# Kernel tuning notes

Hardware: AMD Instinct MI355X
Metric: run time of the kernel (lower is better)

Reference implementation:

```python
import jax, jax.numpy as jnp
import numpy as np

D_MODEL = 512
NUM_HEADS = 8
D_QKV = D_MODEL // NUM_HEADS  # 64
CAPACITY = 2  # EUNN tunable-style rotation layers per step
B = 2
L = 256


def setup_inputs() -> dict:
    key = jax.random.key(0)
    ks = jax.random.split(key, 16)
    f = jnp.float32
    x_q = jax.random.normal(ks[0], (B, L, D_MODEL), f)
    x_k = jax.random.normal(ks[1], (B, L, D_MODEL), f)
    x_v = jax.random.normal(ks[2], (B, L, D_MODEL), f)
    mask = jnp.zeros((B, 1, L, L), f)
    s = 1.0 / np.sqrt(D_MODEL).astype(np.float32)
    Wq = jax.random.normal(ks[3], (D_MODEL, D_MODEL), f) * s
    Wk = jax.random.normal(ks[4], (D_MODEL, D_MODEL), f) * s
    Wv = jax.random.normal(ks[5], (D_MODEL, D_MODEL), f) * s
    Wo = jax.random.normal(ks[6], (D_MODEL, D_MODEL), f) * s
    bq = jnp.zeros((D_MODEL,), f); bk = jnp.zeros((D_MODEL,), f)
    bv = jnp.zeros((D_MODEL,), f); bo = jnp.zeros((D_MODEL,), f)
    pi = np.float32(np.pi)
    theta = jax.random.uniform(ks[7], (NUM_HEADS, CAPACITY, D_QKV // 2), f, -pi, pi)
    phi = jax.random.uniform(ks[8], (NUM_HEADS, CAPACITY, D_QKV // 2), f, -pi, pi)
    sw = 1.0 / np.sqrt(D_QKV).astype(np.float32)
    Win_re = jax.random.normal(ks[9], (NUM_HEADS, D_QKV, D_QKV), f) * sw
    Win_im = jax.random.normal(ks[10], (NUM_HEADS, D_QKV, D_QKV), f) * sw
    rnn_bias = jax.random.normal(ks[11], (NUM_HEADS, D_QKV), f) * 0.01
    return dict(x_q=x_q, x_k=x_k, x_v=x_v, mask=mask, Wq=Wq, bq=bq, Wk=Wk, bk=bk,
                Wv=Wv, bv=bv, Wo=Wo, bo=bo, theta=theta, phi=phi,
                Win_re=Win_re, Win_im=Win_im, rnn_bias=rnn_bias)


def _apply_unitary(h, theta, phi):
    # h: [B,H,Q,d] complex64. EUNN unitary = product of Givens-rotation layers,
    # alternating even pairings (0,1),(2,3),.. and odd pairings via roll.
    for c in range(theta.shape[1]):
        if c % 2 == 1:
            h = jnp.roll(h, -1, axis=-1)
        sh = h.shape
        hp = h.reshape(sh[:-1] + (sh[-1] // 2, 2))
        a, b = hp[..., 0], hp[..., 1]
        cs = jnp.cos(theta[:, c, :])[None, :, None, :]
        sn = jnpp_sin = jnp.sin(theta[:, c, :])[None, :, None, :]
        ph = jnp.exp(1j * phi[:, c, :].astype(jnp.complex64))[None, :, None, :]
        na = cs * a - (sn * ph) * b
        nb = (sn * jnp.conj(ph)) * a + cs * b
        h = jnp.stack([na, nb], axis=-1).reshape(sh)
        if c % 2 == 1:
            h = jnp.roll(h, 1, axis=-1)
    return h


def _modrelu(z, b):
    m = jnp.abs(z)
    scale = jax.nn.relu(m + b) / (m + 1e-5)
    return z * scale.astype(z.dtype)


def _forward(x_q, x_k, x_v, mask, Wq, bq, Wk, bk, Wv, bv, Wo, bo,
             theta, phi, Win_re, Win_im, rnn_bias):
    Bm, Lq, _ = x_q.shape
    def heads(x):
        return x.reshape(Bm, -1, NUM_HEADS, D_QKV).transpose(0, 2, 1, 3)
    q = heads(x_q @ Wq + bq)   # [B,H,Lq,d]
    k = heads(x_k @ Wk + bk)   # [B,H,Lk,d]
    v = heads(x_v @ Wv + bv)   # [B,H,Lk,d]
    logits = jnp.einsum('bhqd,bhkd->bhqk', q, k) / jnp.sqrt(jnp.float32(D_QKV))
    logits = logits - jnp.where(mask == 1.0, jnp.inf, mask)
    attn = jax.nn.softmax(logits, axis=-1)  # [B,H,Lq,Lk]
    Win = (Win_re + 1j * Win_im).astype(jnp.complex64)  # [H,d,d]
    bb = rnn_bias[None, :, None, :]
    def step(h, xs):
        a_t, v_t = xs                              # [B,H,Q], [B,H,d]
        x_t = a_t[..., None] * v_t[:, :, None, :]  # [B,H,Q,d] streamed weighted value
        wx = jnp.einsum('bhqd,hde->bhqe', x_t.astype(jnp.complex64), Win)
        return _modrelu(_apply_unitary(h, theta, phi) + wx, bb), None
    h0 = jnp.zeros((Bm, NUM_HEADS, Lq, D_QKV), jnp.complex64)
    xs = (attn.transpose(3, 0, 1, 2), v.transpose(2, 0, 1, 3))
    hT, _ = jax.lax.scan(step, h0, xs)
    rnn_out = jnp.real(hT)  # [B,H,Lq,d] -- TF takes final RNN state, real part
    out = rnn_out.transpose(0, 2, 1, 3).reshape(Bm, Lq, D_MODEL) @ Wo + bo
    return out, attn


def reference(x_q, x_k, x_v, mask, Wq, bq, Wk, bk, Wv, bv, Wo, bo,
              theta, phi, Win_re, Win_im, rnn_bias):
    return _forward(x_q, x_k, x_v, mask, Wq, bq, Wk, bk, Wv, bv, Wo, bo,
                    theta, phi, Win_re, Win_im, rnn_bias)
```

## Files before the change

### kernel.cpp

```cpp
#include <hip/hip_runtime.h>
#include <math.h>

#define NB 2
#define NL 256
#define DM 512
#define NH 8
#define DQ 64

typedef float v2f __attribute__((ext_vector_type(2)));

#if __has_builtin(__builtin_elementwise_fma)
__device__ __forceinline__ v2f fmav(v2f a, v2f b, v2f c) {
    return __builtin_elementwise_fma(a, b, c);
}
#else
__device__ __forceinline__ v2f fmav(v2f a, v2f b, v2f c) {
    v2f r; r.x = fmaf(a.x, b.x, c.x); r.y = fmaf(a.y, b.y, c.y); return r;
}
#endif
__device__ __forceinline__ v2f swapv(v2f a) {
    return __builtin_shufflevector(a, a, 1, 0);
}

__global__ __launch_bounds__(256) void qkv_gemm(
    const float* __restrict__ xq, const float* __restrict__ xk,
    const float* __restrict__ xv,
    const float* __restrict__ Wq, const float* __restrict__ Wk,
    const float* __restrict__ Wv,
    const float* __restrict__ bq, const float* __restrict__ bk,
    const float* __restrict__ bv,
    const float* __restrict__ Wre, const float* __restrict__ Wim,
    float* __restrict__ q, float* __restrict__ kT, float2* __restrict__ u)
{
    int z = blockIdx.z;
    const float* X = (z == 0) ? xq : (z == 1) ? xk : xv;
    const float* W = (z == 0) ? Wq : (z == 1) ? Wk : Wv;
    const float* bias = (z == 0) ? bq : (z == 1) ? bk : bv;

    __shared__ float As[32][33];
    __shared__ float Bs[32][68];

    int tid = threadIdx.x;
    int tx = tid & 15, ty = tid >> 4;
    int m0 = blockIdx.y * 32, n0 = blockIdx.x * 64;

    int ar = tid >> 3, ac4 = (tid & 7) * 4;
    int br = tid >> 4, bc4 = (tid & 15) * 4;
    const float* Aptr = X + (m0 + ar) * 512 + ac4;
    const float* Bptr0 = W + br * 512 + n0 + bc4;
    const float* Bptr1 = W + (br + 16) * 512 + n0 + bc4;

    float acc[2][4] = {};

    float4 aR = *(const float4*)(Aptr);
    float4 bR0 = *(const float4*)(Bptr0);
    float4 bR1 = *(const float4*)(Bptr1);

    for (int k0 = 0; k0 < 512; k0 += 32) {
        As[ac4 + 0][ar] = aR.x; As[ac4 + 1][ar] = aR.y;
        As[ac4 + 2][ar] = aR.z; As[ac4 + 3][ar] = aR.w;
        *(float4*)&Bs[br][bc4] = bR0;
        *(float4*)&Bs[br + 16][bc4] = bR1;
        __syncthreads();

        if (k0 + 32 < 512) {
            aR  = *(const float4*)(Aptr + k0 + 32);
            bR0 = *(const float4*)(Bptr0 + (k0 + 32) * 512);
            bR1 = *(const float4*)(Bptr1 + (k0 + 32) * 512);
        }

        #pragma unroll
        for (int kk = 0; kk < 32; kk++) {
            float a0 = As[kk][ty * 2 + 0];
            float a1 = As[kk][ty * 2 + 1];
            float4 bb = *(const float4*)&Bs[kk][tx * 4];
            acc[0][0] += a0 * bb.x; acc[0][1] += a0 * bb.y;
            acc[0][2] += a0 * bb.z; acc[0][3] += a0 * bb.w;
            acc[1][0] += a1 * bb.x; acc[1][1] += a1 * bb.y;
            acc[1][2] += a1 * bb.z; acc[1][3] += a1 * bb.w;
        }
        __syncthreads();
    }

    if (z < 2) {
        float* O = (z == 0) ? q : kT;
        #pragma unroll
        for (int i = 0; i < 2; i++) {
            int m = m0 + ty * 2 + i;
            int b = m >> 8, l = m & 255;
            #pragma unroll
            for (int j = 0; j < 4; j++) {
                int n = n0 + tx * 4 + j;
                int h = n >> 6, d = n & 63;
                float val = acc[i][j] + bias[n];
                if (z == 1)
                    O[((b * NH + h) * DQ + d) * NL + l] = val;
                else
                    O[((b * NH + h) * NL + l) * DQ + d] = val;
            }
        }
    } else {
        int h = blockIdx.x;
        int b = m0 >> 8;
        #pragma unroll
        for (int i = 0; i < 2; i++)
            #pragma unroll
            for (int j = 0; j < 4; j++)
                Bs[ty * 2 + i][tx * 4 + j] = acc[i][j] + bias[n0 + tx * 4 + j];
        __syncthreads();

        int r0 = ty * 2, c4 = tx * 4;
        float ur[2][4] = {}, ui[2][4] = {};
        const float* wr = Wre + h * 4096 + c4;
        const float* wi = Wim + h * 4096 + c4;
        #pragma unroll 4
        for (int d = 0; d < 64; d++) {
            float v0 = Bs[r0][d];
            float v1 = Bs[r0 + 1][d];
            float4 wre = *(const float4*)(wr + d * 64);
            float4 wim = *(const float4*)(wi + d * 64);
            ur[0][0] += v0 * wre.x; ur[0][1] += v0 * wre.y;
            ur[0][2] += v0 * wre.z; ur[0][3] += v0 * wre.w;
            ui[0][0] += v0 * wim.x; ui[0][1] += v0 * wim.y;
            ui[0][2] += v0 * wim.z; ui[0][3] += v0 * wim.w;
            ur[1][0] += v1 * wre.x; ur[1][1] += v1 * wre.y;
            ur[1][2] += v1 * wre.z; ur[1][3] += v1 * wre.w;
            ui[1][0] += v1 * wim.x; ui[1][1] += v1 * wim.y;
            ui[1][2] += v1 * wim.z; ui[1][3] += v1 * wim.w;
        }
        #pragma unroll
        for (int i = 0; i < 2; i++) {
            int l = (m0 & 255) + r0 + i;
            float2* up = u + ((size_t)(b * NH + h) * NL + l) * DQ + c4;
            #pragma unroll
            for (int j = 0; j < 4; j++)
                up[j] = make_float2(ur[i][j], ui[i][j]);
        }
    }
}

__device__ __forceinline__ float dpp_swap1(float x) {
    return __int_as_float(__builtin_amdgcn_mov_dpp(__float_as_int(x), 0xB1, 0xF, 0xF, true));
}
__device__ __forceinline__ float dpp_rol1(float x) {
    return __int_as_float(__builtin_amdgcn_mov_dpp(__float_as_int(x), 0x134, 0xF, 0xF, true));
}
__device__ __forceinline__ float dpp_ror1(float x) {
    return __int_as_float(__builtin_amdgcn_mov_dpp(__float_as_int(x), 0x13C, 0xF, 0xF, true));
}

__global__ __launch_bounds__(256) void rnn_kernel(
    const float* __restrict__ q, const float* __restrict__ kT,
    const float* __restrict__ mask, float* __restrict__ attn_o,
    const float2* __restrict__ u,
    const float* __restrict__ theta, const float* __restrict__ phi,
    const float* __restrict__ rnn_bias, float* __restrict__ rnn_out)
{
    int tid  = threadIdx.x;
    int wv   = tid >> 6;
    int lane = tid & 63;

    int blk = blockIdx.x;
    int qg  = blk & 63;
    int h   = (blk >> 6) & 7;
    int b   = blk >> 9;

    __shared__ float qs[256];
    __shared__ float lg[4 * 260];
    __shared__ float redm[4], reds[4];
    __shared__ float arow[4 * 256];

    {
        qs[tid] = q[((size_t)(b * NH + h) * NL + qg * 4) * DQ + tid];
        __syncthreads();

        const float* kp = kT + (size_t)((b * NH + h) * DQ) * NL + tid;
        float acc[4] = {};
        #pragma unroll
        for (int d4 = 0; d4 < 16; d4++) {
            float kv0 = kp[(d4 * 4 + 0) * NL];
            float kv1 = kp[(d4 * 4 + 1) * NL];
            float kv2 = kp[(d4 * 4 + 2) * NL];
            float kv3 = kp[(d4 * 4 + 3) * NL];
            #pragma unroll
            for (int j = 0; j < 4; j++) {
                const float4 qv = *(const float4*)&qs[j * 64 + d4 * 4];
                acc[j] += qv.x * kv0 + qv.y * kv1 + qv.z * kv2 + qv.w * kv3;
            }
        }
        #pragma unroll
        for (int j = 0; j < 4; j++) {
            float mv = mask[(size_t)(b * NL + qg * 4 + j) * NL + tid];
            acc[j] = acc[j] * 0.125f - ((mv == 1.0f) ? INFINITY : mv);
            lg[j * 260 + tid] = acc[j];
        }
        __syncthreads();
        {
            int j = wv;
            float v0 = lg[j * 260 + lane],       v1 = lg[j * 260 + 64 + lane];
            float v2 = lg[j * 260 + 128 + lane], v3 = lg[j * 260 + 192 + lane];
            float mx = fmaxf(fmaxf(v0, v1), fmaxf(v2, v3));
            #pragma unroll
            for (int o = 32; o; o >>= 1) mx = fmaxf(mx, __shfl_xor(mx, o, 64));
            float s = __expf(v0 - mx) + __expf(v1 - mx) +
                      __expf(v2 - mx) + __expf(v3 - mx);
            #pragma unroll
            for (int o = 32; o; o >>= 1) s += __shfl_xor(s, o, 64);
            if (lane == 0) { redm[j] = mx; reds[j] = s; }
        }
        __syncthreads();
        #pragma unroll
        for (int j = 0; j < 4; j++) {
            float p = __expf(acc[j] - redm[j]) * __builtin_amdgcn_rcpf(reds[j]);
            attn_o[((size_t)(b * NH + h) * NL + qg * 4 + j) * NL + tid] = p;
            arow[j * 256 + tid] = p;
        }
        __syncthreads();
    }

    int d = lane;
    bool odd = d & 1;

    const float* tb = theta + h * 64;
    const float* pb = phi + h * 64;

    int i0 = d >> 1;
    float th0 = tb[i0], ph0 = pb[i0];
    float c0 = cosf(th0), s0 = sinf(th0);
    float W0r = (odd ? s0 : -s0) * cosf(ph0);
    float W0i = -s0 * sinf(ph0);

    int i1 = odd ? (d >> 1) : (((d + 62) & 63) >> 1);
    float th1 = tb[32 + i1], ph1 = pb[32 + i1];
    float c1 = cosf(th1), s1 = sinf(th1);
    float W1r = (odd ? -s1 : s1) * cosf(ph1);
    float W1i = -s1 * sinf(ph1);

    float biasv = rnn_bias[h * 64 + d];

    v2f c0v = {c0, c0}, c1v = {c1, c1};
    v2f W0rV = {W0r, W0r}, W0iN = {-W0i, W0i};
    v2f W1rV = {W1r, W1r}, W1iN = {-W1i, W1i};

    const float* arc = arow + wv * 256;
    const float2* up = u + (size_t)((b * NH + h) * NL) * DQ + d;

    v2f e = {0.f, 0.f};
    #pragma unroll 8
    for (int t = 0; t < 256; t++) {
        float2 uu = up[t * 64];
        float a_t = arc[t];
        v2f atv = {a_t, a_t};
        v2f uv = {uu.x, uu.y};

        v2f p0;
        p0.x = dpp_swap1(e.x); p0.y = dpp_swap1(e.y);
        v2f g = fmav(c0v, e, fmav(W0rV, p0, W0iN * swapv(p0)));

        v2f rl, rr;
        rl.x = dpp_rol1(g.x); rl.y = dpp_rol1(g.y);
        rr.x = dpp_ror1(g.x); rr.y = dpp_ror1(g.y);
        v2f p1;
        p1.x = odd ? rl.x : rr.x;
        p1.y = odd ? rl.y : rr.y;

        v2f z = fmav(c1v, g, fmav(W1rV, p1, fmav(W1iN, swapv(p1), atv * uv)));

        float mm = z.x * z.x + z.y * z.y;
        float m = __builtin_amdgcn_sqrtf(mm);
        float sc = fmaxf(m + biasv, 0.f) * __builtin_amdgcn_rcpf(m + 1e-5f);
        v2f scv = {sc, sc};
        e = z * scv;
    }

    int qi = qg * 4 + wv;
    rnn_out[(size_t)(b * NL + qi) * DM + h * DQ + d] = e.x;
}

__global__ __launch_bounds__(256) void out_gemm(
    const float* __restrict__ A, const float* __restrict__ W,
    const float* __restrict__ bias, float* __restrict__ C)
{
    __shared__ float As[32][17];
    __shared__ float Bs[32][68];

    int tid = threadIdx.x;
    int tx = tid & 15, ty = tid >> 4;
    int m0 = blockIdx.y * 16, n0 = blockIdx.x * 64;

    int ar = tid >> 4, ac2 = (tid & 15) * 2;
    int br = tid >> 4, bc4 = (tid & 15) * 4;
    const float* Aptr = A + (m0 + ar) * 512 + ac2;
    const float* Bptr0 = W + br * 512 + n0 + bc4;
    const float* Bptr1 = W + (br + 16) * 512 + n0 + bc4;

    float acc[4] = {};

    float2 aR = *(const float2*)(Aptr);
    float4 bR0 = *(const float4*)(Bptr0);
    float4 bR1 = *(const float4*)(Bptr1);

    for (int k0 = 0; k0 < 512; k0 += 32) {
        As[ac2 + 0][ar] = aR.x; As[ac2 + 1][ar] = aR.y;
        *(float4*)&Bs[br][bc4] = bR0;
        *(float4*)&Bs[br + 16][bc4] = bR1;
        __syncthreads();

        if (k0 + 32 < 512) {
            aR  = *(const float2*)(Aptr + k0 + 32);
            bR0 = *(const float4*)(Bptr0 + (k0 + 32) * 512);
            bR1 = *(const float4*)(Bptr1 + (k0 + 32) * 512);
        }

        #pragma unroll
        for (int kk = 0; kk < 32; kk++) {
            float a = As[kk][ty];
            float4 bb = *(const float4*)&Bs[kk][tx * 4];
            acc[0] += a * bb.x; acc[1] += a * bb.y;
            acc[2] += a * bb.z; acc[3] += a * bb.w;
        }
        __syncthreads();
    }

    int m = m0 + ty;
    #pragma unroll
    for (int j = 0; j < 4; j++) {
        int n = n0 + tx * 4 + j;
        C[m * 512 + n] = acc[j] + bias[n];
    }
}

extern "C" void kernel_launch(void* const* d_in, const int* in_sizes, int n_in,
                              void* d_out, int out_size, void* d_ws, size_t ws_size,
                              hipStream_t stream)
{
    const float* x_q  = (const float*)d_in[0];
    const float* x_k  = (const float*)d_in[1];
    const float* x_v  = (const float*)d_in[2];
    const float* mask = (const float*)d_in[3];
    const float* Wq   = (const float*)d_in[4];
    const float* bq   = (const float*)d_in[5];
    const float* Wk   = (const float*)d_in[6];
    const float* bk   = (const float*)d_in[7];
    const float* Wv   = (const float*)d_in[8];
    const float* bv   = (const float*)d_in[9];
    const float* Wo   = (const float*)d_in[10];
    const float* bo   = (const float*)d_in[11];
    const float* theta= (const float*)d_in[12];
    const float* phi  = (const float*)d_in[13];
    const float* Wre  = (const float*)d_in[14];
    const float* Wim  = (const float*)d_in[15];
    const float* rb   = (const float*)d_in[16];

    float* ws = (float*)d_ws;
    float*  q_ws    = ws;
    float*  kT_ws   = ws + 262144;
    float2* u_ws    = (float2*)(ws + 524288);
    float*  rnn_o   = ws + 1048576;

    float* out_o  = (float*)d_out;
    float* attn_o = out_o + NB * NL * DM;

    qkv_gemm<<<dim3(8, 16, 3), 256, 0, stream>>>(
        x_q, x_k, x_v, Wq, Wk, Wv, bq, bk, bv, Wre, Wim,
        q_ws, kT_ws, u_ws);

    rnn_kernel<<<dim3(1024), 256, 0, stream>>>(
        q_ws, kT_ws, mask, attn_o, u_ws, theta, phi, rb, rnn_o);

    out_gemm<<<dim3(8, 32), 256, 0, stream>>>(rnn_o, Wo, bo, out_o);
}
```

Measured before the change: 188.5 us.

## Pack four hidden dims per lane in RNN scan with 64-thread blocks

The RNN kernel now uses one 64-lane wavefront per block, and each lane holds four consecutive hidden dimensions of one query row (16 lanes per row, 4 rows per wave). The first Givens layer becomes purely in-register, so only one row-rotate DPP per boundary is needed instead of the previous swap plus two rotates. The attention softmax is computed by the single wave with no cross-wave reductions. Per-step u values and attention weights are double-buffered as float4 register loads to hide latency. The cost is fewer threads per CU (256 threads become 64 per block) and more registers per lane, so occupancy and latency hiding depend on how many blocks fit.

```diff
diff --git a/kernel.cpp b/kernel.cpp
--- a/kernel.cpp
+++ b/kernel.cpp
@@ -139,142 +139,183 @@
     }
 }
 
-__device__ __forceinline__ float dpp_swap1(float x) {
-    return __int_as_float(__builtin_amdgcn_mov_dpp(__float_as_int(x), 0xB1, 0xF, 0xF, true));
-}
-__device__ __forceinline__ float dpp_rol1(float x) {
-    return __int_as_float(__builtin_amdgcn_mov_dpp(__float_as_int(x), 0x134, 0xF, 0xF, true));
-}
-__device__ __forceinline__ float dpp_ror1(float x) {
-    return __int_as_float(__builtin_amdgcn_mov_dpp(__float_as_int(x), 0x13C, 0xF, 0xF, true));
-}
-
-__global__ __launch_bounds__(256) void rnn_kernel(
+__device__ __forceinline__ float dpp_row_ror1(float x) {
+    return __int_as_float(__builtin_amdgcn_mov_dpp(__float_as_int(x), 0x121, 0xF, 0xF, true));
+}
+__device__ __forceinline__ float dpp_row_rol1(float x) {
+    return __int_as_float(__builtin_amdgcn_mov_dpp(__float_as_int(x), 0x12F, 0xF, 0xF, true));
+}
+
+__device__ __forceinline__ v2f mdr(v2f z, float bv) {
+    float mm = z.x * z.x + z.y * z.y;
+    float m = __builtin_amdgcn_sqrtf(mm);
+    float sc = fmaxf(m + bv, 0.f) * __builtin_amdgcn_rcpf(m + 1e-5f);
+    v2f s = {sc, sc};
+    return z * s;
+}
+
+__global__ __launch_bounds__(64) void rnn_kernel(
     const float* __restrict__ q, const float* __restrict__ kT,
     const float* __restrict__ mask, float* __restrict__ attn_o,
     const float2* __restrict__ u,
     const float* __restrict__ theta, const float* __restrict__ phi,
     const float* __restrict__ rnn_bias, float* __restrict__ rnn_out)
 {
-    int tid  = threadIdx.x;
-    int wv   = tid >> 6;
-    int lane = tid & 63;
-
+    int lane = threadIdx.x;
     int blk = blockIdx.x;
-    int qg  = blk & 63;
-    int h   = (blk >> 6) & 7;
-    int b   = blk >> 9;
-
-    __shared__ float qs[256];
-    __shared__ float lg[4 * 260];
-    __shared__ float redm[4], reds[4];
-    __shared__ float arow[4 * 256];
+    int qg = blk & 63;
+    int h  = (blk >> 6) & 7;
+    int b  = blk >> 9;
+
+    int row = lane >> 4;
+    int p   = lane & 15;
+
+    __shared__ float qs[4][68];
+    __shared__ float arow[4][260];
 
     {
-        qs[tid] = q[((size_t)(b * NH + h) * NL + qg * 4) * DQ + tid];
-        __syncthreads();
-
-        const float* kp = kT + (size_t)((b * NH + h) * DQ) * NL + tid;
-        float acc[4] = {};
+        const float4* qsrc = (const float4*)(q + ((size_t)(b * NH + h) * NL + qg * 4) * DQ);
+        float4 f4 = qsrc[lane];
+        *(float4*)&qs[lane >> 4][(lane & 15) * 4] = f4;
+    }
+    __syncthreads();
+
+    float l[4][4];
+    {
+        const float* kp = kT + (size_t)((b * NH + h) * DQ) * NL + lane;
+        float acc[4][4] = {};
         #pragma unroll
         for (int d4 = 0; d4 < 16; d4++) {
-            float kv0 = kp[(d4 * 4 + 0) * NL];
-            float kv1 = kp[(d4 * 4 + 1) * NL];
-            float kv2 = kp[(d4 * 4 + 2) * NL];
-            float kv3 = kp[(d4 * 4 + 3) * NL];
-            #pragma unroll
-            for (int j = 0; j < 4; j++) {
-                const float4 qv = *(const float4*)&qs[j * 64 + d4 * 4];
-                acc[j] += qv.x * kv0 + qv.y * kv1 + qv.z * kv2 + qv.w * kv3;
+            float kv[4][4];
+            #pragma unroll
+            for (int kk = 0; kk < 4; kk++)
+                #pragma unroll
+                for (int i = 0; i < 4; i++)
+                    kv[kk][i] = kp[(size_t)(d4 * 4 + i) * NL + kk * 64];
+            #pragma unroll
+            for (int r = 0; r < 4; r++) {
+                float4 qv = *(const float4*)&qs[r][d4 * 4];
+                #pragma unroll
+                for (int kk = 0; kk < 4; kk++)
+                    acc[r][kk] += qv.x * kv[kk][0] + qv.y * kv[kk][1]
+                                + qv.z * kv[kk][2] + qv.w * kv[kk][3];
             }
         }
         #pragma unroll
-        for (int j = 0; j < 4; j++) {
-            float mv = mask[(size_t)(b * NL + qg * 4 + j) * NL + tid];
-            acc[j] = acc[j] * 0.125f - ((mv == 1.0f) ? INFINITY : mv);
-            lg[j * 260 + tid] = acc[j];
-        }
-        __syncthreads();
-        {
-            int j = wv;
-            float v0 = lg[j * 260 + lane],       v1 = lg[j * 260 + 64 + lane];
-            float v2 = lg[j * 260 + 128 + lane], v3 = lg[j * 260 + 192 + lane];
-            float mx = fmaxf(fmaxf(v0, v1), fmaxf(v2, v3));
+        for (int r = 0; r < 4; r++)
+            #pragma unroll
+            for (int kk = 0; kk < 4; kk++) {
+                float mv = mask[(size_t)(b * NL + qg * 4 + r) * NL + lane + kk * 64];
+                l[r][kk] = acc[r][kk] * 0.125f - ((mv == 1.0f) ? INFINITY : mv);
+            }
+        #pragma unroll
+        for (int r = 0; r < 4; r++) {
+            float mx = fmaxf(fmaxf(l[r][0], l[r][1]), fmaxf(l[r][2], l[r][3]));
             #pragma unroll
             for (int o = 32; o; o >>= 1) mx = fmaxf(mx, __shfl_xor(mx, o, 64));
-            float s = __expf(v0 - mx) + __expf(v1 - mx) +
-                      __expf(v2 - mx) + __expf(v3 - mx);
+            float s = __expf(l[r][0] - mx) + __expf(l[r][1] - mx)
+                    + __expf(l[r][2] - mx) + __expf(l[r][3] - mx);
             #pragma unroll
             for (int o = 32; o; o >>= 1) s += __shfl_xor(s, o, 64);
-            if (lane == 0) { redm[j] = mx; reds[j] = s; }
-        }
-        __syncthreads();
-        #pragma unroll
-        for (int j = 0; j < 4; j++) {
-            float p = __expf(acc[j] - redm[j]) * __builtin_amdgcn_rcpf(reds[j]);
-            attn_o[((size_t)(b * NH + h) * NL + qg * 4 + j) * NL + tid] = p;
-            arow[j * 256 + tid] = p;
-        }
-        __syncthreads();
-    }
-
-    int d = lane;
-    bool odd = d & 1;
+            float rs = __builtin_amdgcn_rcpf(s);
+            #pragma unroll
+            for (int kk = 0; kk < 4; kk++) {
+                float pv = __expf(l[r][kk] - mx) * rs;
+                attn_o[((size_t)(b * NH + h) * NL + qg * 4 + r) * NL + lane + kk * 64] = pv;
+                arow[r][lane + kk * 64] = pv;
+            }
+        }
+    }
+    __syncthreads();
 
     const float* tb = theta + h * 64;
     const float* pb = phi + h * 64;
 
-    int i0 = d >> 1;
-    float th0 = tb[i0], ph0 = pb[i0];
-    float c0 = cosf(th0), s0 = sinf(th0);
-    float W0r = (odd ? s0 : -s0) * cosf(ph0);
-    float W0i = -s0 * sinf(ph0);
-
-    int i1 = odd ? (d >> 1) : (((d + 62) & 63) >> 1);
-    float th1 = tb[32 + i1], ph1 = pb[32 + i1];
-    float c1 = cosf(th1), s1 = sinf(th1);
-    float W1r = (odd ? -s1 : s1) * cosf(ph1);
-    float W1i = -s1 * sinf(ph1);
-
-    float biasv = rnn_bias[h * 64 + d];
-
-    v2f c0v = {c0, c0}, c1v = {c1, c1};
-    v2f W0rV = {W0r, W0r}, W0iN = {-W0i, W0i};
-    v2f W1rV = {W1r, W1r}, W1iN = {-W1i, W1i};
-
-    const float* arc = arow + wv * 256;
-    const float2* up = u + (size_t)((b * NH + h) * NL) * DQ + d;
-
-    v2f e = {0.f, 0.f};
-    #pragma unroll 8
-    for (int t = 0; t < 256; t++) {
-        float2 uu = up[t * 64];
-        float a_t = arc[t];
-        v2f atv = {a_t, a_t};
-        v2f uv = {uu.x, uu.y};
-
-        v2f p0;
-        p0.x = dpp_swap1(e.x); p0.y = dpp_swap1(e.y);
-        v2f g = fmav(c0v, e, fmav(W0rV, p0, W0iN * swapv(p0)));
-
-        v2f rl, rr;
-        rl.x = dpp_rol1(g.x); rl.y = dpp_rol1(g.y);
-        rr.x = dpp_ror1(g.x); rr.y = dpp_ror1(g.y);
-        v2f p1;
-        p1.x = odd ? rl.x : rr.x;
-        p1.y = odd ? rl.y : rr.y;
-
-        v2f z = fmav(c1v, g, fmav(W1rV, p1, fmav(W1iN, swapv(p1), atv * uv)));
-
-        float mm = z.x * z.x + z.y * z.y;
-        float m = __builtin_amdgcn_sqrtf(mm);
-        float sc = fmaxf(m + biasv, 0.f) * __builtin_amdgcn_rcpf(m + 1e-5f);
-        v2f scv = {sc, sc};
-        e = z * scv;
-    }
-
-    int qi = qg * 4 + wv;
-    rnn_out[(size_t)(b * NL + qi) * DM + h * DQ + d] = e.x;
+    float thA = tb[2 * p], phA = pb[2 * p];
+    float cA = cosf(thA), sA = sinf(thA), cpA = cosf(phA), spA = sinf(phA);
+    float thB = tb[2 * p + 1], phB = pb[2 * p + 1];
+    float cB = cosf(thB), sB = sinf(thB), cpB = cosf(phB), spB = sinf(phB);
+
+    #define MKC(nm, Wr, Wi) v2f nm##rV = {(Wr), (Wr)}; v2f nm##iN = {-(Wi), (Wi)}
+    MKC(WAa, -sA * cpA, -sA * spA);
+    MKC(WAb,  sA * cpA, -sA * spA);
+    MKC(WBa, -sB * cpB, -sB * spB);
+    MKC(WBb,  sB * cpB, -sB * spB);
+    v2f cAv = {cA, cA}, cBv = {cB, cB};
+
+    int iL = (2 * p + 31) & 31;
+    float thL = tb[32 + iL], phL = pb[32 + iL];
+    float cL = cosf(thL), sL = sinf(thL);
+    MKC(W1L,  sL * cosf(phL), -sL * sinf(phL));
+    float thM = tb[32 + 2 * p], phM = pb[32 + 2 * p];
+    float cM = cosf(thM), sM = sinf(thM), cpM = cosf(phM), spM = sinf(phM);
+    MKC(W1M, -sM * cpM, -sM * spM);
+    MKC(W2M,  sM * cpM, -sM * spM);
+    float thR = tb[32 + 2 * p + 1], phR = pb[32 + 2 * p + 1];
+    float cR = cosf(thR), sR = sinf(thR);
+    MKC(W1R, -sR * cosf(phR), -sR * sinf(phR));
+    v2f cLv = {cL, cL}, cMv = {cM, cM}, cRv = {cR, cR};
+    #undef MKC
+
+    float4 bias4 = *(const float4*)&rnn_bias[h * 64 + 4 * p];
+
+    v2f e0 = {0.f, 0.f}, e1 = {0.f, 0.f}, e2 = {0.f, 0.f}, e3 = {0.f, 0.f};
+
+    #define STEP(a_t, uA, uB) do {                                           \
+        v2f atv = {(a_t), (a_t)};                                            \
+        v2f u0 = {(uA).x, (uA).y}, u1 = {(uA).z, (uA).w};                    \
+        v2f u2 = {(uB).x, (uB).y}, u3 = {(uB).z, (uB).w};                    \
+        v2f g0 = fmav(cAv, e0, fmav(WAarV, e1, WAaiN * swapv(e1)));          \
+        v2f g1 = fmav(cAv, e1, fmav(WAbrV, e0, WAbiN * swapv(e0)));          \
+        v2f g2 = fmav(cBv, e2, fmav(WBarV, e3, WBaiN * swapv(e3)));          \
+        v2f g3 = fmav(cBv, e3, fmav(WBbrV, e2, WBbiN * swapv(e2)));          \
+        v2f gl, gr;                                                          \
+        gl.x = dpp_row_ror1(g3.x); gl.y = dpp_row_ror1(g3.y);                \
+        gr.x = dpp_row_rol1(g0.x); gr.y = dpp_row_rol1(g0.y);                \
+        v2f z0 = fmav(cLv, g0, fmav(W1LrV, gl, fmav(W1LiN, swapv(gl), atv * u0))); \
+        v2f z1 = fmav(cMv, g1, fmav(W1MrV, g2, fmav(W1MiN, swapv(g2), atv * u1))); \
+        v2f z2 = fmav(cMv, g2, fmav(W2MrV, g1, fmav(W2MiN, swapv(g1), atv * u2))); \
+        v2f z3 = fmav(cRv, g3, fmav(W1RrV, gr, fmav(W1RiN, swapv(gr), atv * u3))); \
+        e0 = mdr(z0, bias4.x); e1 = mdr(z1, bias4.y);                        \
+        e2 = mdr(z2, bias4.z); e3 = mdr(z3, bias4.w);                        \
+    } while (0)
+
+    const float4* up4 = (const float4*)(u + (size_t)((b * NH + h) * NL) * DQ) + 2 * p;
+
+    float4 Ua[8], Ub[8];
+    float4 aa, ab;
+    #pragma unroll
+    for (int i = 0; i < 8; i++) Ua[i] = up4[(i >> 1) * 32 + (i & 1)];
+    aa = *(const float4*)&arow[row][0];
+
+    for (int c = 0; c < 64; c += 2) {
+        const float4* upn = up4 + (c + 1) * 128;
+        #pragma unroll
+        for (int i = 0; i < 8; i++) Ub[i] = upn[(i >> 1) * 32 + (i & 1)];
+        ab = *(const float4*)&arow[row][(c + 1) * 4];
+
+        STEP(aa.x, Ua[0], Ua[1]);
+        STEP(aa.y, Ua[2], Ua[3]);
+        STEP(aa.z, Ua[4], Ua[5]);
+        STEP(aa.w, Ua[6], Ua[7]);
+
+        if (c + 2 < 64) {
+            const float4* upn2 = up4 + (c + 2) * 128;
+            #pragma unroll
+            for (int i = 0; i < 8; i++) Ua[i] = upn2[(i >> 1) * 32 + (i & 1)];
+            aa = *(const float4*)&arow[row][(c + 2) * 4];
+        }
+
+        STEP(ab.x, Ub[0], Ub[1]);
+        STEP(ab.y, Ub[2], Ub[3]);
+        STEP(ab.z, Ub[4], Ub[5]);
+        STEP(ab.w, Ub[6], Ub[7]);
+    }
+    #undef STEP
+
+    int qi = qg * 4 + row;
+    float4 o4 = {e0.x, e1.x, e2.x, e3.x};
+    *(float4*)&rnn_out[(size_t)(b * NL + qi) * DM + h * DQ + 4 * p] = o4;
 }
 
 __global__ __launch_bounds__(256) void out_gemm(
@@ -365,7 +406,7 @@
         x_q, x_k, x_v, Wq, Wk, Wv, bq, bk, bv, Wre, Wim,
         q_ws, kT_ws, u_ws);
 
-    rnn_kernel<<<dim3(1024), 256, 0, stream>>>(
+    rnn_kernel<<<dim3(1024), 64, 0, stream>>>(
         q_ws, kT_ws, mask, attn_o, u_ws, theta, phi, rb, rnn_o);
 
     out_gemm<<<dim3(8, 32), 256, 0, stream>>>(rnn_o, Wo, bo, out_o);
```

New measurement: 182.0 us. -3.5%, faster.

## Split attention softmax into its own kernel and double-buffer RNN loads

Applied to the files above, without the earlier changes.

Moves the QK^T/softmax computation out of the RNN kernel into a separate one-wave-per-block attention kernel, so the RNN kernel reads attention rows from global memory instead of shared memory. The RNN recurrence loop now prefetches the u and attention values for the next 8 steps into registers while computing the current 8, so global load latency is hidden behind the serial dependency chain. It also adds a launch-bounds occupancy hint. The cost is an extra kernel launch, a round trip of the attention matrix through memory, and more register use.

```diff
diff --git a/kernel.cpp b/kernel.cpp
--- a/kernel.cpp
+++ b/kernel.cpp
@@ -139,6 +139,70 @@
     }
 }
 
+__global__ __launch_bounds__(64) void attn_kernel(
+    const float* __restrict__ q, const float* __restrict__ kT,
+    const float* __restrict__ mask, float* __restrict__ attn_o)
+{
+    int lane = threadIdx.x;
+    int blk = blockIdx.x;
+    int qg = blk & 63;
+    int h  = (blk >> 6) & 7;
+    int b  = blk >> 9;
+
+    __shared__ float qs[4][68];
+
+    {
+        const float4* qsrc = (const float4*)(q + ((size_t)(b * NH + h) * NL + qg * 4) * DQ);
+        float4 f4 = qsrc[lane];
+        *(float4*)&qs[lane >> 4][(lane & 15) * 4] = f4;
+    }
+    __syncthreads();
+
+    const float* kp = kT + (size_t)((b * NH + h) * DQ) * NL + lane;
+    float acc[4][4] = {};
+    #pragma unroll
+    for (int d4 = 0; d4 < 16; d4++) {
+        float kv[4][4];
+        #pragma unroll
+        for (int kk = 0; kk < 4; kk++)
+            #pragma unroll
+            for (int i = 0; i < 4; i++)
+                kv[kk][i] = kp[(size_t)(d4 * 4 + i) * NL + kk * 64];
+        #pragma unroll
+        for (int r = 0; r < 4; r++) {
+            float4 qv = *(const float4*)&qs[r][d4 * 4];
+            #pragma unroll
+            for (int kk = 0; kk < 4; kk++)
+                acc[r][kk] += qv.x * kv[kk][0] + qv.y * kv[kk][1]
+                            + qv.z * kv[kk][2] + qv.w * kv[kk][3];
+        }
+    }
+    float l[4][4];
+    #pragma unroll
+    for (int r = 0; r < 4; r++)
+        #pragma unroll
+        for (int kk = 0; kk < 4; kk++) {
+            float mv = mask[(size_t)(b * NL + qg * 4 + r) * NL + lane + kk * 64];
+            l[r][kk] = acc[r][kk] * 0.125f - ((mv == 1.0f) ? INFINITY : mv);
+        }
+    #pragma unroll
+    for (int r = 0; r < 4; r++) {
+        float mx = fmaxf(fmaxf(l[r][0], l[r][1]), fmaxf(l[r][2], l[r][3]));
+        #pragma unroll
+        for (int o = 32; o; o >>= 1) mx = fmaxf(mx, __shfl_xor(mx, o, 64));
+        float s = __expf(l[r][0] - mx) + __expf(l[r][1] - mx)
+                + __expf(l[r][2] - mx) + __expf(l[r][3] - mx);
+        #pragma unroll
+        for (int o = 32; o; o >>= 1) s += __shfl_xor(s, o, 64);
+        float rs = __builtin_amdgcn_rcpf(s);
+        #pragma unroll
+        for (int kk = 0; kk < 4; kk++) {
+            float pv = __expf(l[r][kk] - mx) * rs;
+            attn_o[((size_t)(b * NH + h) * NL + qg * 4 + r) * NL + lane + kk * 64] = pv;
+        }
+    }
+}
+
 __device__ __forceinline__ float dpp_swap1(float x) {
     return __int_as_float(__builtin_amdgcn_mov_dpp(__float_as_int(x), 0xB1, 0xF, 0xF, true));
 }
@@ -149,74 +213,27 @@
     return __int_as_float(__builtin_amdgcn_mov_dpp(__float_as_int(x), 0x13C, 0xF, 0xF, true));
 }
 
-__global__ __launch_bounds__(256) void rnn_kernel(
-    const float* __restrict__ q, const float* __restrict__ kT,
-    const float* __restrict__ mask, float* __restrict__ attn_o,
-    const float2* __restrict__ u,
+__device__ __forceinline__ v2f mdr(v2f z, float bv) {
+    float mm = z.x * z.x + z.y * z.y;
+    float m = __builtin_amdgcn_sqrtf(mm);
+    float sc = fmaxf(m + bv, 0.f) * __builtin_amdgcn_rcpf(m + 1e-5f);
+    v2f s = {sc, sc};
+    return z * s;
+}
+
+__global__ __launch_bounds__(256, 4) void rnn_kernel(
+    const float* __restrict__ attn, const float2* __restrict__ u,
     const float* __restrict__ theta, const float* __restrict__ phi,
     const float* __restrict__ rnn_bias, float* __restrict__ rnn_out)
 {
     int tid  = threadIdx.x;
+    int lane = tid & 63;
     int wv   = tid >> 6;
-    int lane = tid & 63;
-
-    int blk = blockIdx.x;
-    int qg  = blk & 63;
-    int h   = (blk >> 6) & 7;
-    int b   = blk >> 9;
-
-    __shared__ float qs[256];
-    __shared__ float lg[4 * 260];
-    __shared__ float redm[4], reds[4];
-    __shared__ float arow[4 * 256];
-
-    {
-        qs[tid] = q[((size_t)(b * NH + h) * NL + qg * 4) * DQ + tid];
-        __syncthreads();
-
-        const float* kp = kT + (size_t)((b * NH + h) * DQ) * NL + tid;
-        float acc[4] = {};
-        #pragma unroll
-        for (int d4 = 0; d4 < 16; d4++) {
-            float kv0 = kp[(d4 * 4 + 0) * NL];
-            float kv1 = kp[(d4 * 4 + 1) * NL];
-            float kv2 = kp[(d4 * 4 + 2) * NL];
-            float kv3 = kp[(d4 * 4 + 3) * NL];
-            #pragma unroll
-            for (int j = 0; j < 4; j++) {
-                const float4 qv = *(const float4*)&qs[j * 64 + d4 * 4];
-                acc[j] += qv.x * kv0 + qv.y * kv1 + qv.z * kv2 + qv.w * kv3;
-            }
-        }
-        #pragma unroll
-        for (int j = 0; j < 4; j++) {
-            float mv = mask[(size_t)(b * NL + qg * 4 + j) * NL + tid];
-            acc[j] = acc[j] * 0.125f - ((mv == 1.0f) ? INFINITY : mv);
-            lg[j * 260 + tid] = acc[j];
-        }
-        __syncthreads();
-        {
-            int j = wv;
-            float v0 = lg[j * 260 + lane],       v1 = lg[j * 260 + 64 + lane];
-            float v2 = lg[j * 260 + 128 + lane], v3 = lg[j * 260 + 192 + lane];
-            float mx = fmaxf(fmaxf(v0, v1), fmaxf(v2, v3));
-            #pragma unroll
-            for (int o = 32; o; o >>= 1) mx = fmaxf(mx, __shfl_xor(mx, o, 64));
-            float s = __expf(v0 - mx) + __expf(v1 - mx) +
-                      __expf(v2 - mx) + __expf(v3 - mx);
-            #pragma unroll
-            for (int o = 32; o; o >>= 1) s += __shfl_xor(s, o, 64);
-            if (lane == 0) { redm[j] = mx; reds[j] = s; }
-        }
-        __syncthreads();
-        #pragma unroll
-        for (int j = 0; j < 4; j++) {
-            float p = __expf(acc[j] - redm[j]) * __builtin_amdgcn_rcpf(reds[j]);
-            attn_o[((size_t)(b * NH + h) * NL + qg * 4 + j) * NL + tid] = p;
-            arow[j * 256 + tid] = p;
-        }
-        __syncthreads();
-    }
+    int blk  = blockIdx.x;
+    int qg   = blk & 63;
+    int h    = (blk >> 6) & 7;
+    int b    = blk >> 9;
+    int qi   = qg * 4 + wv;
 
     int d = lane;
     bool odd = d & 1;
@@ -242,38 +259,58 @@
     v2f W0rV = {W0r, W0r}, W0iN = {-W0i, W0i};
     v2f W1rV = {W1r, W1r}, W1iN = {-W1i, W1i};
 
-    const float* arc = arow + wv * 256;
+    const float* ar = attn + ((size_t)(b * NH + h) * NL + qi) * NL;
     const float2* up = u + (size_t)((b * NH + h) * NL) * DQ + d;
 
     v2f e = {0.f, 0.f};
-    #pragma unroll 8
-    for (int t = 0; t < 256; t++) {
-        float2 uu = up[t * 64];
-        float a_t = arc[t];
-        v2f atv = {a_t, a_t};
-        v2f uv = {uu.x, uu.y};
-
-        v2f p0;
-        p0.x = dpp_swap1(e.x); p0.y = dpp_swap1(e.y);
-        v2f g = fmav(c0v, e, fmav(W0rV, p0, W0iN * swapv(p0)));
-
-        v2f rl, rr;
-        rl.x = dpp_rol1(g.x); rl.y = dpp_rol1(g.y);
-        rr.x = dpp_ror1(g.x); rr.y = dpp_ror1(g.y);
-        v2f p1;
-        p1.x = odd ? rl.x : rr.x;
-        p1.y = odd ? rl.y : rr.y;
-
-        v2f z = fmav(c1v, g, fmav(W1rV, p1, fmav(W1iN, swapv(p1), atv * uv)));
-
-        float mm = z.x * z.x + z.y * z.y;
-        float m = __builtin_amdgcn_sqrtf(mm);
-        float sc = fmaxf(m + biasv, 0.f) * __builtin_amdgcn_rcpf(m + 1e-5f);
-        v2f scv = {sc, sc};
-        e = z * scv;
-    }
-
-    int qi = qg * 4 + wv;
+
+    #define RSTEP(a_t, uu) do {                                              \
+        v2f atv = {(a_t), (a_t)};                                            \
+        v2f uv = {(uu).x, (uu).y};                                           \
+        v2f p0;                                                              \
+        p0.x = dpp_swap1(e.x); p0.y = dpp_swap1(e.y);                        \
+        v2f g = fmav(c0v, e, fmav(W0rV, p0, W0iN * swapv(p0)));              \
+        v2f rl, rr;                                                          \
+        rl.x = dpp_rol1(g.x); rl.y = dpp_rol1(g.y);                          \
+        rr.x = dpp_ror1(g.x); rr.y = dpp_ror1(g.y);                          \
+        v2f p1;                                                              \
+        p1.x = odd ? rl.x : rr.x;                                            \
+        p1.y = odd ? rl.y : rr.y;                                            \
+        v2f z = fmav(c1v, g, fmav(W1rV, p1, fmav(W1iN, swapv(p1), atv * uv))); \
+        e = mdr(z, biasv);                                                   \
+    } while (0)
+
+    float2 A0[8], A1[8];
+    float  s0v[8], s1v[8];
+
+    #pragma unroll
+    for (int i = 0; i < 8; i++) A0[i] = up[i * 64];
+    #pragma unroll
+    for (int i = 0; i < 8; i++) s0v[i] = ar[i];
+
+    for (int k = 0; k < 16; k++) {
+        int t1 = k * 16 + 8;
+        #pragma unroll
+        for (int i = 0; i < 8; i++) A1[i] = up[(t1 + i) * 64];
+        #pragma unroll
+        for (int i = 0; i < 8; i++) s1v[i] = ar[t1 + i];
+
+        #pragma unroll
+        for (int j = 0; j < 8; j++) RSTEP(s0v[j], A0[j]);
+
+        if (k < 15) {
+            int t2 = k * 16 + 16;
+            #pragma unroll
+            for (int i = 0; i < 8; i++) A0[i] = up[(t2 + i) * 64];
+            #pragma unroll
+            for (int i = 0; i < 8; i++) s0v[i] = ar[t2 + i];
+        }
+
+        #pragma unroll
+        for (int j = 0; j < 8; j++) RSTEP(s1v[j], A1[j]);
+    }
+    #undef RSTEP
+
     rnn_out[(size_t)(b * NL + qi) * DM + h * DQ + d] = e.x;
 }
 
@@ -365,8 +402,11 @@
         x_q, x_k, x_v, Wq, Wk, Wv, bq, bk, bv, Wre, Wim,
         q_ws, kT_ws, u_ws);
 
+    attn_kernel<<<dim3(1024), 64, 0, stream>>>(
+        q_ws, kT_ws, mask, attn_o);
+
     rnn_kernel<<<dim3(1024), 256, 0, stream>>>(
-        q_ws, kT_ws, mask, attn_o, u_ws, theta, phi, rb, rnn_o);
+        attn_o, u_ws, theta, phi, rb, rnn_o);
 
     out_gemm<<<dim3(8, 32), 256, 0, stream>>>(rnn_o, Wo, bo, out_o);
 }
```

New measurement: 198.7 us. 1.05x slower.
